# Kernel optimization log

Measured on AMD Instinct MI355X. Metric: run time of the kernel, lower is better.

The kernel has to match this reference:

```python
import jax, jax.numpy as jnp
import numpy as np

BETA = 0.25


def setup_inputs() -> dict:
    key = jax.random.key(0)
    k1, k2 = jax.random.split(key)
    B, W, H, C = 32, 64, 64, 64
    K = 512
    x = jax.random.normal(k1, (B, W, H, C), dtype=jnp.float32)
    # original uses random_uniform_initializer(0, 1)
    embedding = jax.random.uniform(k2, (K, C), dtype=jnp.float32)
    return {"x": x, "embedding": embedding}


def reference(x, embedding):
    B, W, H, C = x.shape
    K = embedding.shape[0]
    flat = x.reshape(-1, C)  # (N, C), N = B*W*H
    # squared L2 distance, expanded form (same math as sum((flat - emb)^2, -1))
    # avoids materializing the (N, K, C) tiled tensor of the original
    x2 = jnp.sum(flat * flat, axis=-1, keepdims=True)          # (N, 1)
    e2 = jnp.sum(embedding * embedding, axis=-1)               # (K,)
    cross = jnp.einsum('nc,kc->nk', flat, embedding)           # (N, K)
    dist = x2 - 2.0 * cross + e2[None, :]                      # (N, K)
    idx = jnp.argmin(dist, axis=-1).reshape(B, W, H)           # (B, W, H)
    quantized = embedding[idx]                                 # (B, W, H, C)
    embedding_loss = jnp.mean((jax.lax.stop_gradient(x) - quantized) ** 2)
    encoding_loss = jnp.mean((x - jax.lax.stop_gradient(quantized)) ** 2)
    loss = embedding_loss + BETA * encoding_loss
    # straight-through estimator
    quantized_ste = x + jax.lax.stop_gradient(quantized - x)
    return quantized_ste, loss
```

## Files before the change

kernel.cpp:

```cpp
#include <hip/hip_runtime.h>


#define C_DIM 64
#define K_EMB 512
#define NVEC (32 * 64 * 64)
#define BLK 512
#define VPW 64
#define NPB 512
#define GRID (NVEC / NPB)
#define KT (K_EMB / 16)
#define NT 4

typedef __attribute__((ext_vector_type(8))) short bf16x8;
typedef __attribute__((ext_vector_type(4))) float f32x4;

#define WS_E2   0
#define WS_EHI  4096
#define WS_ELO  (4096 + 65536)
#define WS_PART (4096 + 2 * 65536)

__device__ inline unsigned short f2bf(float f) {
    unsigned u = __float_as_uint(f);
    u += 0x7FFF + ((u >> 16) & 1);
    return (unsigned short)(u >> 16);
}
__device__ inline float bf2f(unsigned short h) {
    return __uint_as_float(((unsigned)h) << 16);
}
__device__ inline bool lessidx(float s, int i, float t, int j) {
    return (s < t) || (s == t && i < j);
}

__global__ __launch_bounds__(512) void vq_prep(const float* __restrict__ emb,
                                               float* __restrict__ e2,
                                               short* __restrict__ ehi,
                                               short* __restrict__ elo) {
    const int t = blockIdx.x * 512 + threadIdx.x;
    const int l = t & 63;
    const int kt2 = t >> 6;
    const int row = (kt2 >> 1) * 16 + (l & 15);
    const int cb  = (kt2 & 1) * 32 + (l >> 4) * 8;
    const float* src = emb + row * C_DIM + cb;
    bf16x8 vh, vl;
#pragma unroll
    for (int j = 0; j < 8; ++j) {
        float v = -2.0f * src[j];
        unsigned short h = f2bf(v);
        float hf = bf2f(h);
        unsigned short q = f2bf(v - hf);
        vh[j] = (short)h;
        vl[j] = (short)q;
    }
    *(bf16x8*)(ehi + (size_t)t * 8) = vh;
    *(bf16x8*)(elo + (size_t)t * 8) = vl;

    if (t < K_EMB) {
        const float* r = emb + t * C_DIM;
        float s = 0.f;
#pragma unroll
        for (int c = 0; c < C_DIM; ++c) s += r[c] * r[c];
        e2[t] = s;
    }
}

__global__ __launch_bounds__(BLK, 2) void vq_main(
    const float* __restrict__ x,
    const float* __restrict__ emb,
    const float* __restrict__ e2g,
    const short* __restrict__ ehi_g,
    const short* __restrict__ elo_g,
    float* __restrict__ out,
    double* __restrict__ partials)
{
    __shared__ __align__(16) short s_hi[K_EMB * C_DIM];
    __shared__ __align__(16) short s_lo[K_EMB * C_DIM];
    __shared__ __align__(16) float s_e2[K_EMB];
    __shared__ double s_wsum[BLK / 64];

    const int tid = threadIdx.x;

    {
        const float4* srch = (const float4*)ehi_g;
        const float4* srcl = (const float4*)elo_g;
        float4* dsth = (float4*)s_hi;
        float4* dstl = (float4*)s_lo;
#pragma unroll
        for (int i = 0; i < 16; ++i) dsth[tid + i * BLK] = srch[tid + i * BLK];
#pragma unroll
        for (int i = 0; i < 16; ++i) dstl[tid + i * BLK] = srcl[tid + i * BLK];
        if (tid < K_EMB) s_e2[tid] = e2g[tid];
    }
    __syncthreads();

    const int lane = tid & 63;
    const int wid  = tid >> 6;
    const int lr   = lane & 15;
    const int lh   = lane >> 4;
    const int nbase = blockIdx.x * NPB + wid * VPW;

    bf16x8 xh[NT][2], xl[NT][2];
    float x2p[NT];
#pragma unroll
    for (int nt = 0; nt < NT; ++nt) {
        const int n = nbase + nt * 16 + lr;
        const float* xp = x + (size_t)n * C_DIM;
        x2p[nt] = 0.f;
#pragma unroll
        for (int s = 0; s < 2; ++s) {
            const float* p = xp + s * 32 + lh * 8;
            float4 a = *(const float4*)(p);
            float4 b = *(const float4*)(p + 4);
            float vv[8] = {a.x, a.y, a.z, a.w, b.x, b.y, b.z, b.w};
#pragma unroll
            for (int j = 0; j < 8; ++j) {
                float v = vv[j];
                x2p[nt] += v * v;
                unsigned short h = f2bf(v);
                float hf = bf2f(h);
                unsigned short q = f2bf(v - hf);
                xh[nt][s][j] = (short)h;
                xl[nt][s][j] = (short)q;
            }
        }
    }

    float pb1[NT], pb2[NT];
#pragma unroll
    for (int nt = 0; nt < NT; ++nt) { pb1[nt] = 1e30f; pb2[nt] = 1e30f; }

    for (int kt = 0; kt < KT; ++kt) {
        const bf16x8* hp = (const bf16x8*)s_hi + kt * 128 + lane;
        const bf16x8* lp = (const bf16x8*)s_lo + kt * 128 + lane;
        bf16x8 ah0 = hp[0], ah1 = hp[64];
        bf16x8 al0 = lp[0], al1 = lp[64];
        float4 ev = *(const float4*)(s_e2 + kt * 16 + lh * 4);
        f32x4 a0 = {ev.x, ev.y, ev.z, ev.w};
        f32x4 a1 = a0, a2 = a0, a3 = a0;

        a0 = __builtin_amdgcn_mfma_f32_16x16x32_bf16(ah0, xh[0][0], a0, 0, 0, 0);
        a1 = __builtin_amdgcn_mfma_f32_16x16x32_bf16(ah0, xh[1][0], a1, 0, 0, 0);
        a2 = __builtin_amdgcn_mfma_f32_16x16x32_bf16(ah0, xh[2][0], a2, 0, 0, 0);
        a3 = __builtin_amdgcn_mfma_f32_16x16x32_bf16(ah0, xh[3][0], a3, 0, 0, 0);
        a0 = __builtin_amdgcn_mfma_f32_16x16x32_bf16(ah1, xh[0][1], a0, 0, 0, 0);
        a1 = __builtin_amdgcn_mfma_f32_16x16x32_bf16(ah1, xh[1][1], a1, 0, 0, 0);
        a2 = __builtin_amdgcn_mfma_f32_16x16x32_bf16(ah1, xh[2][1], a2, 0, 0, 0);
        a3 = __builtin_amdgcn_mfma_f32_16x16x32_bf16(ah1, xh[3][1], a3, 0, 0, 0);
        a0 = __builtin_amdgcn_mfma_f32_16x16x32_bf16(al0, xh[0][0], a0, 0, 0, 0);
        a1 = __builtin_amdgcn_mfma_f32_16x16x32_bf16(al0, xh[1][0], a1, 0, 0, 0);
        a2 = __builtin_amdgcn_mfma_f32_16x16x32_bf16(al0, xh[2][0], a2, 0, 0, 0);
        a3 = __builtin_amdgcn_mfma_f32_16x16x32_bf16(al0, xh[3][0], a3, 0, 0, 0);
        a0 = __builtin_amdgcn_mfma_f32_16x16x32_bf16(al1, xh[0][1], a0, 0, 0, 0);
        a1 = __builtin_amdgcn_mfma_f32_16x16x32_bf16(al1, xh[1][1], a1, 0, 0, 0);
        a2 = __builtin_amdgcn_mfma_f32_16x16x32_bf16(al1, xh[2][1], a2, 0, 0, 0);
        a3 = __builtin_amdgcn_mfma_f32_16x16x32_bf16(al1, xh[3][1], a3, 0, 0, 0);
        a0 = __builtin_amdgcn_mfma_f32_16x16x32_bf16(ah0, xl[0][0], a0, 0, 0, 0);
        a1 = __builtin_amdgcn_mfma_f32_16x16x32_bf16(ah0, xl[1][0], a1, 0, 0, 0);
        a2 = __builtin_amdgcn_mfma_f32_16x16x32_bf16(ah0, xl[2][0], a2, 0, 0, 0);
        a3 = __builtin_amdgcn_mfma_f32_16x16x32_bf16(ah0, xl[3][0], a3, 0, 0, 0);
        a0 = __builtin_amdgcn_mfma_f32_16x16x32_bf16(ah1, xl[0][1], a0, 0, 0, 0);
        a1 = __builtin_amdgcn_mfma_f32_16x16x32_bf16(ah1, xl[1][1], a1, 0, 0, 0);
        a2 = __builtin_amdgcn_mfma_f32_16x16x32_bf16(ah1, xl[2][1], a2, 0, 0, 0);
        a3 = __builtin_amdgcn_mfma_f32_16x16x32_bf16(ah1, xl[3][1], a3, 0, 0, 0);

        const unsigned kb4 = (unsigned)(kt * 4);
#define PACKMIN(ACC, NTI)                                                          \
        {                                                                          \
            unsigned q0 = ((__float_as_uint(ACC[0]) + 64u) & 0xFFFFFF80u) | (kb4 + 0); \
            unsigned q1 = ((__float_as_uint(ACC[1]) + 64u) & 0xFFFFFF80u) | (kb4 + 1); \
            unsigned q2 = ((__float_as_uint(ACC[2]) + 64u) & 0xFFFFFF80u) | (kb4 + 2); \
            unsigned q3 = ((__float_as_uint(ACC[3]) + 64u) & 0xFFFFFF80u) | (kb4 + 3); \
            float f0 = __uint_as_float(q0), f1 = __uint_as_float(q1);              \
            float f2 = __uint_as_float(q2), f3 = __uint_as_float(q3);              \
            float lo = fminf(f0, f1), hi = fmaxf(f0, f1);                          \
            pb2[NTI] = fminf(fminf(pb2[NTI], fmaxf(pb1[NTI], lo)), hi);            \
            pb1[NTI] = fminf(pb1[NTI], lo);                                        \
            lo = fminf(f2, f3); hi = fmaxf(f2, f3);                                \
            pb2[NTI] = fminf(fminf(pb2[NTI], fmaxf(pb1[NTI], lo)), hi);            \
            pb1[NTI] = fminf(pb1[NTI], lo);                                        \
        }
        PACKMIN(a0, 0)
        PACKMIN(a1, 1)
        PACKMIN(a2, 2)
        PACKMIN(a3, 3)
#undef PACKMIN
    }

    double dsum = 0.0;
#pragma unroll
    for (int nt = 0; nt < NT; ++nt) {
        unsigned u1 = __float_as_uint(pb1[nt]);
        unsigned u2 = __float_as_uint(pb2[nt]);
        int loc1 = u1 & 127, loc2 = u2 & 127;
        float b1 = __uint_as_float(u1 & 0xFFFFFF80u);
        float b2 = __uint_as_float(u2 & 0xFFFFFF80u);
        int i1 = ((loc1 >> 2) << 4) + lh * 4 + (loc1 & 3);
        int i2 = ((loc2 >> 2) << 4) + lh * 4 + (loc2 & 3);
        float xx = x2p[nt];
#pragma unroll
        for (int off = 16; off <= 32; off <<= 1) {
            float ob1 = __shfl_xor(b1, off, 64);
            int   oi1 = __shfl_xor(i1, off, 64);
            float ob2 = __shfl_xor(b2, off, 64);
            int   oi2 = __shfl_xor(i2, off, 64);
            float oxx = __shfl_xor(xx, off, 64);
            xx += oxx;
            bool to = lessidx(ob1, oi1, b1, i1);
            float w1 = to ? ob1 : b1;  int wi1 = to ? oi1 : i1;
            float l1 = to ? b1 : ob1;  int li1 = to ? i1 : oi1;
            float c2 = to ? ob2 : b2;  int ci2 = to ? oi2 : i2;
            bool t2 = lessidx(l1, li1, c2, ci2);
            b1 = w1; i1 = wi1;
            b2 = t2 ? l1 : c2; i2 = t2 ? li1 : ci2;
        }

        int bw = i1;
        if (lane < 16) {
            double md;
            if (b2 - b1 < 1.2e-2f) {
                const int n = nbase + nt * 16 + lane;
                const float4* xq = (const float4*)(x + (size_t)n * C_DIM);
                const float4* p1 = (const float4*)(emb + (size_t)i1 * C_DIM);
                const float4* p2 = (const float4*)(emb + (size_t)i2 * C_DIM);
                double s1 = 0.0, s2 = 0.0;
#pragma unroll
                for (int i = 0; i < 16; ++i) {
                    float4 xv = xq[i]; float4 a = p1[i]; float4 bq = p2[i];
                    double d;
                    d = (double)xv.x - (double)a.x;  s1 = fma(d, d, s1);
                    d = (double)xv.y - (double)a.y;  s1 = fma(d, d, s1);
                    d = (double)xv.z - (double)a.z;  s1 = fma(d, d, s1);
                    d = (double)xv.w - (double)a.w;  s1 = fma(d, d, s1);
                    d = (double)xv.x - (double)bq.x; s2 = fma(d, d, s2);
                    d = (double)xv.y - (double)bq.y; s2 = fma(d, d, s2);
                    d = (double)xv.z - (double)bq.z; s2 = fma(d, d, s2);
                    d = (double)xv.w - (double)bq.w; s2 = fma(d, d, s2);
                }
                if (s2 < s1 || (s1 == s2 && i2 < i1)) { bw = i2; md = s2; }
                else                                   { md = s1; }
            } else {
                md = (double)xx + (double)b1;
            }
            dsum += md;
        }

        {
            const int v  = lane >> 2;
            const int c0 = lane & 3;
            const int w  = __shfl(bw, v);
            const size_t rowb = ((size_t)(nbase + nt * 16 + v)) * 16;
            const float4* ep = (const float4*)emb + (size_t)w * 16;
            float4* op = (float4*)out;
#pragma unroll
            for (int it = 0; it < 4; ++it) op[rowb + c0 + it * 4] = ep[c0 + it * 4];
        }
    }

#pragma unroll
    for (int off = 1; off <= 8; off <<= 1) dsum += __shfl_xor(dsum, off, 64);
    if (lane == 0) s_wsum[wid] = dsum;
    __syncthreads();
    if (tid == 0) {
        double t = 0.0;
#pragma unroll
        for (int i = 0; i < BLK / 64; ++i) t += s_wsum[i];
        partials[blockIdx.x] = t;
    }
}

__global__ __launch_bounds__(256) void vq_finalize(const double* __restrict__ partials,
                                                   float* __restrict__ out) {
    double v = partials[threadIdx.x];
#pragma unroll
    for (int off = 32; off; off >>= 1) v += __shfl_down(v, off, 64);
    __shared__ double ls[4];
    const int lane = threadIdx.x & 63;
    const int wid  = threadIdx.x >> 6;
    if (lane == 0) ls[wid] = v;
    __syncthreads();
    if (threadIdx.x == 0) {
        double t = ls[0] + ls[1] + ls[2] + ls[3];
        double mean = t / (double)((size_t)NVEC * C_DIM);
        out[(size_t)NVEC * C_DIM] = (float)(1.25 * mean);
    }
}

extern "C" void kernel_launch(void* const* d_in, const int* in_sizes, int n_in,
                              void* d_out, int out_size, void* d_ws, size_t ws_size,
                              hipStream_t stream) {
    const float* x   = (const float*)d_in[0];
    const float* emb = (const float*)d_in[1];
    float* out = (float*)d_out;

    float*  e2       = (float*)((char*)d_ws + WS_E2);
    short*  ehi      = (short*)((char*)d_ws + WS_EHI);
    short*  elo      = (short*)((char*)d_ws + WS_ELO);
    double* partials = (double*)((char*)d_ws + WS_PART);

    vq_prep<<<8, 512, 0, stream>>>(emb, e2, ehi, elo);
    vq_main<<<GRID, BLK, 0, stream>>>(x, emb, e2, ehi, elo, out, partials);
    vq_finalize<<<1, 256, 0, stream>>>(partials, out);
}
```

Baseline: 51.83 us.

## Split per-wave vectors into two batches and prefetch the next batch and fragments

Each wave now handles its 64 vectors as two batches of 32 (NT=2), reusing the same k-loop and epilogue twice. The first batch's x rows are loaded before the codebook is staged into LDS, and the second batch's rows are loaded while the first batch is computed, so global load latency overlaps with work. The k-loop double-buffers the LDS codebook fragments one step ahead and is partially unrolled. The LDS staging loop is also cut from 16 to 8 iterations, which matches the shared-array size. This lowers accumulator register use, at the cost of reading the codebook fragments from LDS twice.

```diff
diff --git a/kernel.cpp b/kernel.cpp
--- a/kernel.cpp
+++ b/kernel.cpp
@@ -5,11 +5,11 @@
 #define K_EMB 512
 #define NVEC (32 * 64 * 64)
 #define BLK 512
-#define VPW 64
 #define NPB 512
+#define NBAT 256
 #define GRID (NVEC / NPB)
 #define KT (K_EMB / 16)
-#define NT 4
+#define NT 2
 
 typedef __attribute__((ext_vector_type(8))) short bf16x8;
 typedef __attribute__((ext_vector_type(4))) float f32x4;
@@ -63,53 +63,16 @@
     }
 }
 
-__global__ __launch_bounds__(BLK, 2) void vq_main(
-    const float* __restrict__ x,
-    const float* __restrict__ emb,
-    const float* __restrict__ e2g,
-    const short* __restrict__ ehi_g,
-    const short* __restrict__ elo_g,
-    float* __restrict__ out,
-    double* __restrict__ partials)
-{
-    __shared__ __align__(16) short s_hi[K_EMB * C_DIM];
-    __shared__ __align__(16) short s_lo[K_EMB * C_DIM];
-    __shared__ __align__(16) float s_e2[K_EMB];
-    __shared__ double s_wsum[BLK / 64];
-
-    const int tid = threadIdx.x;
-
-    {
-        const float4* srch = (const float4*)ehi_g;
-        const float4* srcl = (const float4*)elo_g;
-        float4* dsth = (float4*)s_hi;
-        float4* dstl = (float4*)s_lo;
-#pragma unroll
-        for (int i = 0; i < 16; ++i) dsth[tid + i * BLK] = srch[tid + i * BLK];
-#pragma unroll
-        for (int i = 0; i < 16; ++i) dstl[tid + i * BLK] = srcl[tid + i * BLK];
-        if (tid < K_EMB) s_e2[tid] = e2g[tid];
-    }
-    __syncthreads();
-
-    const int lane = tid & 63;
-    const int wid  = tid >> 6;
-    const int lr   = lane & 15;
-    const int lh   = lane >> 4;
-    const int nbase = blockIdx.x * NPB + wid * VPW;
-
-    bf16x8 xh[NT][2], xl[NT][2];
-    float x2p[NT];
+__device__ __forceinline__ void make_frags(const float4 xr[8],
+                                           bf16x8 xh[NT][2], bf16x8 xl[NT][2],
+                                           float x2p[NT]) {
 #pragma unroll
     for (int nt = 0; nt < NT; ++nt) {
-        const int n = nbase + nt * 16 + lr;
-        const float* xp = x + (size_t)n * C_DIM;
         x2p[nt] = 0.f;
 #pragma unroll
         for (int s = 0; s < 2; ++s) {
-            const float* p = xp + s * 32 + lh * 8;
-            float4 a = *(const float4*)(p);
-            float4 b = *(const float4*)(p + 4);
+            float4 a = xr[nt * 4 + s * 2 + 0];
+            float4 b = xr[nt * 4 + s * 2 + 1];
             float vv[8] = {a.x, a.y, a.z, a.w, b.x, b.y, b.z, b.w};
 #pragma unroll
             for (int j = 0; j < 8; ++j) {
@@ -123,44 +86,47 @@
             }
         }
     }
-
-    float pb1[NT], pb2[NT];
+}
+
+__device__ __forceinline__ void kloop(const short* s_hi, const short* s_lo,
+                                      const float* s_e2, int lane, int lh,
+                                      const bf16x8 xh[NT][2], const bf16x8 xl[NT][2],
+                                      float pb1[NT], float pb2[NT]) {
+    const bf16x8* hb = (const bf16x8*)s_hi + lane;
+    const bf16x8* lb = (const bf16x8*)s_lo + lane;
+    bf16x8 ah0 = hb[0], ah1 = hb[64];
+    bf16x8 al0 = lb[0], al1 = lb[64];
+    float4 ev = *(const float4*)(s_e2 + lh * 4);
+
 #pragma unroll
     for (int nt = 0; nt < NT; ++nt) { pb1[nt] = 1e30f; pb2[nt] = 1e30f; }
 
+#pragma unroll 4
     for (int kt = 0; kt < KT; ++kt) {
-        const bf16x8* hp = (const bf16x8*)s_hi + kt * 128 + lane;
-        const bf16x8* lp = (const bf16x8*)s_lo + kt * 128 + lane;
-        bf16x8 ah0 = hp[0], ah1 = hp[64];
-        bf16x8 al0 = lp[0], al1 = lp[64];
-        float4 ev = *(const float4*)(s_e2 + kt * 16 + lh * 4);
+        bf16x8 nh0 = ah0, nh1 = ah1, nl0 = al0, nl1 = al1;
+        float4 nev = ev;
+        if (kt + 1 < KT) {
+            nh0 = hb[(kt + 1) * 128];
+            nh1 = hb[(kt + 1) * 128 + 64];
+            nl0 = lb[(kt + 1) * 128];
+            nl1 = lb[(kt + 1) * 128 + 64];
+            nev = *(const float4*)(s_e2 + (kt + 1) * 16 + lh * 4);
+        }
+
         f32x4 a0 = {ev.x, ev.y, ev.z, ev.w};
-        f32x4 a1 = a0, a2 = a0, a3 = a0;
-
+        f32x4 a1 = a0;
         a0 = __builtin_amdgcn_mfma_f32_16x16x32_bf16(ah0, xh[0][0], a0, 0, 0, 0);
         a1 = __builtin_amdgcn_mfma_f32_16x16x32_bf16(ah0, xh[1][0], a1, 0, 0, 0);
-        a2 = __builtin_amdgcn_mfma_f32_16x16x32_bf16(ah0, xh[2][0], a2, 0, 0, 0);
-        a3 = __builtin_amdgcn_mfma_f32_16x16x32_bf16(ah0, xh[3][0], a3, 0, 0, 0);
         a0 = __builtin_amdgcn_mfma_f32_16x16x32_bf16(ah1, xh[0][1], a0, 0, 0, 0);
         a1 = __builtin_amdgcn_mfma_f32_16x16x32_bf16(ah1, xh[1][1], a1, 0, 0, 0);
-        a2 = __builtin_amdgcn_mfma_f32_16x16x32_bf16(ah1, xh[2][1], a2, 0, 0, 0);
-        a3 = __builtin_amdgcn_mfma_f32_16x16x32_bf16(ah1, xh[3][1], a3, 0, 0, 0);
         a0 = __builtin_amdgcn_mfma_f32_16x16x32_bf16(al0, xh[0][0], a0, 0, 0, 0);
         a1 = __builtin_amdgcn_mfma_f32_16x16x32_bf16(al0, xh[1][0], a1, 0, 0, 0);
-        a2 = __builtin_amdgcn_mfma_f32_16x16x32_bf16(al0, xh[2][0], a2, 0, 0, 0);
-        a3 = __builtin_amdgcn_mfma_f32_16x16x32_bf16(al0, xh[3][0], a3, 0, 0, 0);
         a0 = __builtin_amdgcn_mfma_f32_16x16x32_bf16(al1, xh[0][1], a0, 0, 0, 0);
         a1 = __builtin_amdgcn_mfma_f32_16x16x32_bf16(al1, xh[1][1], a1, 0, 0, 0);
-        a2 = __builtin_amdgcn_mfma_f32_16x16x32_bf16(al1, xh[2][1], a2, 0, 0, 0);
-        a3 = __builtin_amdgcn_mfma_f32_16x16x32_bf16(al1, xh[3][1], a3, 0, 0, 0);
         a0 = __builtin_amdgcn_mfma_f32_16x16x32_bf16(ah0, xl[0][0], a0, 0, 0, 0);
         a1 = __builtin_amdgcn_mfma_f32_16x16x32_bf16(ah0, xl[1][0], a1, 0, 0, 0);
-        a2 = __builtin_amdgcn_mfma_f32_16x16x32_bf16(ah0, xl[2][0], a2, 0, 0, 0);
-        a3 = __builtin_amdgcn_mfma_f32_16x16x32_bf16(ah0, xl[3][0], a3, 0, 0, 0);
         a0 = __builtin_amdgcn_mfma_f32_16x16x32_bf16(ah1, xl[0][1], a0, 0, 0, 0);
         a1 = __builtin_amdgcn_mfma_f32_16x16x32_bf16(ah1, xl[1][1], a1, 0, 0, 0);
-        a2 = __builtin_amdgcn_mfma_f32_16x16x32_bf16(ah1, xl[2][1], a2, 0, 0, 0);
-        a3 = __builtin_amdgcn_mfma_f32_16x16x32_bf16(ah1, xl[3][1], a3, 0, 0, 0);
 
         const unsigned kb4 = (unsigned)(kt * 4);
 #define PACKMIN(ACC, NTI)                                                          \
@@ -180,11 +146,17 @@
         }
         PACKMIN(a0, 0)
         PACKMIN(a1, 1)
-        PACKMIN(a2, 2)
-        PACKMIN(a3, 3)
 #undef PACKMIN
-    }
-
+        ah0 = nh0; ah1 = nh1; al0 = nl0; al1 = nl1; ev = nev;
+    }
+}
+
+__device__ __forceinline__ double epilogue(const float* __restrict__ x,
+                                           const float* __restrict__ emb,
+                                           float* __restrict__ out,
+                                           int nbase, int lane, int lh,
+                                           const float pb1[NT], const float pb2[NT],
+                                           const float x2p[NT]) {
     double dsum = 0.0;
 #pragma unroll
     for (int nt = 0; nt < NT; ++nt) {
@@ -254,6 +226,78 @@
             for (int it = 0; it < 4; ++it) op[rowb + c0 + it * 4] = ep[c0 + it * 4];
         }
     }
+    return dsum;
+}
+
+__global__ __launch_bounds__(BLK, 2) void vq_main(
+    const float* __restrict__ x,
+    const float* __restrict__ emb,
+    const float* __restrict__ e2g,
+    const short* __restrict__ ehi_g,
+    const short* __restrict__ elo_g,
+    float* __restrict__ out,
+    double* __restrict__ partials)
+{
+    __shared__ __align__(16) short s_hi[K_EMB * C_DIM];
+    __shared__ __align__(16) short s_lo[K_EMB * C_DIM];
+    __shared__ __align__(16) float s_e2[K_EMB];
+    __shared__ double s_wsum[BLK / 64];
+
+    const int tid  = threadIdx.x;
+    const int lane = tid & 63;
+    const int wid  = tid >> 6;
+    const int lr   = lane & 15;
+    const int lh   = lane >> 4;
+    const int nbase0 = blockIdx.x * NPB + wid * 32;
+    const int nbase1 = blockIdx.x * NPB + NBAT + wid * 32;
+
+    float4 xr0[8];
+#pragma unroll
+    for (int nt = 0; nt < NT; ++nt) {
+        const float* xp = x + (size_t)(nbase0 + nt * 16 + lr) * C_DIM;
+#pragma unroll
+        for (int s = 0; s < 2; ++s) {
+            xr0[nt * 4 + s * 2 + 0] = *(const float4*)(xp + s * 32 + lh * 8);
+            xr0[nt * 4 + s * 2 + 1] = *(const float4*)(xp + s * 32 + lh * 8 + 4);
+        }
+    }
+
+    {
+        const float4* srch = (const float4*)ehi_g;
+        const float4* srcl = (const float4*)elo_g;
+        float4* dsth = (float4*)s_hi;
+        float4* dstl = (float4*)s_lo;
+#pragma unroll
+        for (int i = 0; i < 8; ++i) dsth[tid + i * BLK] = srch[tid + i * BLK];
+#pragma unroll
+        for (int i = 0; i < 8; ++i) dstl[tid + i * BLK] = srcl[tid + i * BLK];
+        if (tid < K_EMB) s_e2[tid] = e2g[tid];
+    }
+    __syncthreads();
+
+    bf16x8 xh[NT][2], xl[NT][2];
+    float x2p0[NT];
+    make_frags(xr0, xh, xl, x2p0);
+
+    float4 xr1[8];
+#pragma unroll
+    for (int nt = 0; nt < NT; ++nt) {
+        const float* xp = x + (size_t)(nbase1 + nt * 16 + lr) * C_DIM;
+#pragma unroll
+        for (int s = 0; s < 2; ++s) {
+            xr1[nt * 4 + s * 2 + 0] = *(const float4*)(xp + s * 32 + lh * 8);
+            xr1[nt * 4 + s * 2 + 1] = *(const float4*)(xp + s * 32 + lh * 8 + 4);
+        }
+    }
+
+    float pb1[NT], pb2[NT];
+    kloop(s_hi, s_lo, s_e2, lane, lh, xh, xl, pb1, pb2);
+    double dsum = epilogue(x, emb, out, nbase0, lane, lh, pb1, pb2, x2p0);
+
+    float x2p1[NT];
+    make_frags(xr1, xh, xl, x2p1);
+    kloop(s_hi, s_lo, s_e2, lane, lh, xh, xl, pb1, pb2);
+    dsum += epilogue(x, emb, out, nbase1, lane, lh, pb1, pb2, x2p1);
 
 #pragma unroll
     for (int off = 1; off <= 8; off <<= 1) dsum += __shfl_xor(dsum, off, 64);
```

After: 50.66 us. 1.02x faster.

## Halve codebook LDS footprint via two-chunk staging and raise occupancy

Applied to the files above, without the earlier changes.

Stages the bf16 hi/lo codebook into shared memory in two halves of 256 entries instead of the full 512, cutting LDS per block from about 130KB to about 66KB. Each block now covers 256 vectors (2 tiles per wave), launch bounds rise to 4, and the grid and finalize kernel double to 512. The x loads are issued before the codebook copy so global latency overlaps it. The MFMA chain is split into three independent accumulators (hi*hi, lo*hi, hi*lo) that are summed at the end to shorten dependency chains. The cost is an extra mid-loop barrier and reload, and the codebook is re-read from global by twice as many blocks.

```diff
diff --git a/kernel.cpp b/kernel.cpp
--- a/kernel.cpp
+++ b/kernel.cpp
@@ -3,13 +3,13 @@
 
 #define C_DIM 64
 #define K_EMB 512
+#define KCH   (K_EMB / 2)
 #define NVEC (32 * 64 * 64)
 #define BLK 512
-#define VPW 64
-#define NPB 512
+#define NPB 256
 #define GRID (NVEC / NPB)
-#define KT (K_EMB / 16)
-#define NT 4
+#define KTC 16
+#define NT 2
 
 typedef __attribute__((ext_vector_type(8))) short bf16x8;
 typedef __attribute__((ext_vector_type(4))) float f32x4;
@@ -63,7 +63,7 @@
     }
 }
 
-__global__ __launch_bounds__(BLK, 2) void vq_main(
+__global__ __launch_bounds__(BLK, 4) void vq_main(
     const float* __restrict__ x,
     const float* __restrict__ emb,
     const float* __restrict__ e2g,
@@ -72,44 +72,51 @@
     float* __restrict__ out,
     double* __restrict__ partials)
 {
-    __shared__ __align__(16) short s_hi[K_EMB * C_DIM];
-    __shared__ __align__(16) short s_lo[K_EMB * C_DIM];
+    __shared__ __align__(16) short s_hi[KCH * C_DIM];
+    __shared__ __align__(16) short s_lo[KCH * C_DIM];
     __shared__ __align__(16) float s_e2[K_EMB];
     __shared__ double s_wsum[BLK / 64];
 
-    const int tid = threadIdx.x;
-
+    const int tid  = threadIdx.x;
+    const int lane = tid & 63;
+    const int wid  = tid >> 6;
+    const int lr   = lane & 15;
+    const int lh   = lane >> 4;
+    const int nbase = blockIdx.x * NPB + wid * 32;
+
+    float4 xr[8];
+#pragma unroll
+    for (int nt = 0; nt < NT; ++nt) {
+        const float* xp = x + (size_t)(nbase + nt * 16 + lr) * C_DIM;
+#pragma unroll
+        for (int s = 0; s < 2; ++s) {
+            xr[nt * 4 + s * 2 + 0] = *(const float4*)(xp + s * 32 + lh * 8);
+            xr[nt * 4 + s * 2 + 1] = *(const float4*)(xp + s * 32 + lh * 8 + 4);
+        }
+    }
+
+    if (tid < K_EMB) s_e2[tid] = e2g[tid];
     {
         const float4* srch = (const float4*)ehi_g;
         const float4* srcl = (const float4*)elo_g;
         float4* dsth = (float4*)s_hi;
         float4* dstl = (float4*)s_lo;
 #pragma unroll
-        for (int i = 0; i < 16; ++i) dsth[tid + i * BLK] = srch[tid + i * BLK];
-#pragma unroll
-        for (int i = 0; i < 16; ++i) dstl[tid + i * BLK] = srcl[tid + i * BLK];
-        if (tid < K_EMB) s_e2[tid] = e2g[tid];
+        for (int i = 0; i < 4; ++i) dsth[tid + i * BLK] = srch[tid + i * BLK];
+#pragma unroll
+        for (int i = 0; i < 4; ++i) dstl[tid + i * BLK] = srcl[tid + i * BLK];
     }
     __syncthreads();
-
-    const int lane = tid & 63;
-    const int wid  = tid >> 6;
-    const int lr   = lane & 15;
-    const int lh   = lane >> 4;
-    const int nbase = blockIdx.x * NPB + wid * VPW;
 
     bf16x8 xh[NT][2], xl[NT][2];
     float x2p[NT];
 #pragma unroll
     for (int nt = 0; nt < NT; ++nt) {
-        const int n = nbase + nt * 16 + lr;
-        const float* xp = x + (size_t)n * C_DIM;
         x2p[nt] = 0.f;
 #pragma unroll
         for (int s = 0; s < 2; ++s) {
-            const float* p = xp + s * 32 + lh * 8;
-            float4 a = *(const float4*)(p);
-            float4 b = *(const float4*)(p + 4);
+            float4 a = xr[nt * 4 + s * 2 + 0];
+            float4 b = xr[nt * 4 + s * 2 + 1];
             float vv[8] = {a.x, a.y, a.z, a.w, b.x, b.y, b.z, b.w};
 #pragma unroll
             for (int j = 0; j < 8; ++j) {
@@ -124,65 +131,73 @@
         }
     }
 
-    float pb1[NT], pb2[NT];
-#pragma unroll
-    for (int nt = 0; nt < NT; ++nt) { pb1[nt] = 1e30f; pb2[nt] = 1e30f; }
-
-    for (int kt = 0; kt < KT; ++kt) {
-        const bf16x8* hp = (const bf16x8*)s_hi + kt * 128 + lane;
-        const bf16x8* lp = (const bf16x8*)s_lo + kt * 128 + lane;
-        bf16x8 ah0 = hp[0], ah1 = hp[64];
-        bf16x8 al0 = lp[0], al1 = lp[64];
-        float4 ev = *(const float4*)(s_e2 + kt * 16 + lh * 4);
-        f32x4 a0 = {ev.x, ev.y, ev.z, ev.w};
-        f32x4 a1 = a0, a2 = a0, a3 = a0;
-
-        a0 = __builtin_amdgcn_mfma_f32_16x16x32_bf16(ah0, xh[0][0], a0, 0, 0, 0);
-        a1 = __builtin_amdgcn_mfma_f32_16x16x32_bf16(ah0, xh[1][0], a1, 0, 0, 0);
-        a2 = __builtin_amdgcn_mfma_f32_16x16x32_bf16(ah0, xh[2][0], a2, 0, 0, 0);
-        a3 = __builtin_amdgcn_mfma_f32_16x16x32_bf16(ah0, xh[3][0], a3, 0, 0, 0);
-        a0 = __builtin_amdgcn_mfma_f32_16x16x32_bf16(ah1, xh[0][1], a0, 0, 0, 0);
-        a1 = __builtin_amdgcn_mfma_f32_16x16x32_bf16(ah1, xh[1][1], a1, 0, 0, 0);
-        a2 = __builtin_amdgcn_mfma_f32_16x16x32_bf16(ah1, xh[2][1], a2, 0, 0, 0);
-        a3 = __builtin_amdgcn_mfma_f32_16x16x32_bf16(ah1, xh[3][1], a3, 0, 0, 0);
-        a0 = __builtin_amdgcn_mfma_f32_16x16x32_bf16(al0, xh[0][0], a0, 0, 0, 0);
-        a1 = __builtin_amdgcn_mfma_f32_16x16x32_bf16(al0, xh[1][0], a1, 0, 0, 0);
-        a2 = __builtin_amdgcn_mfma_f32_16x16x32_bf16(al0, xh[2][0], a2, 0, 0, 0);
-        a3 = __builtin_amdgcn_mfma_f32_16x16x32_bf16(al0, xh[3][0], a3, 0, 0, 0);
-        a0 = __builtin_amdgcn_mfma_f32_16x16x32_bf16(al1, xh[0][1], a0, 0, 0, 0);
-        a1 = __builtin_amdgcn_mfma_f32_16x16x32_bf16(al1, xh[1][1], a1, 0, 0, 0);
-        a2 = __builtin_amdgcn_mfma_f32_16x16x32_bf16(al1, xh[2][1], a2, 0, 0, 0);
-        a3 = __builtin_amdgcn_mfma_f32_16x16x32_bf16(al1, xh[3][1], a3, 0, 0, 0);
-        a0 = __builtin_amdgcn_mfma_f32_16x16x32_bf16(ah0, xl[0][0], a0, 0, 0, 0);
-        a1 = __builtin_amdgcn_mfma_f32_16x16x32_bf16(ah0, xl[1][0], a1, 0, 0, 0);
-        a2 = __builtin_amdgcn_mfma_f32_16x16x32_bf16(ah0, xl[2][0], a2, 0, 0, 0);
-        a3 = __builtin_amdgcn_mfma_f32_16x16x32_bf16(ah0, xl[3][0], a3, 0, 0, 0);
-        a0 = __builtin_amdgcn_mfma_f32_16x16x32_bf16(ah1, xl[0][1], a0, 0, 0, 0);
-        a1 = __builtin_amdgcn_mfma_f32_16x16x32_bf16(ah1, xl[1][1], a1, 0, 0, 0);
-        a2 = __builtin_amdgcn_mfma_f32_16x16x32_bf16(ah1, xl[2][1], a2, 0, 0, 0);
-        a3 = __builtin_amdgcn_mfma_f32_16x16x32_bf16(ah1, xl[3][1], a3, 0, 0, 0);
-
-        const unsigned kb4 = (unsigned)(kt * 4);
+    float pb1[NT] = {1e30f, 1e30f}, pb2[NT] = {1e30f, 1e30f};
+
+#pragma unroll 1
+    for (int ch = 0; ch < 2; ++ch) {
+        if (ch == 1) {
+            __syncthreads();
+            const float4* srch = (const float4*)ehi_g + 2048;
+            const float4* srcl = (const float4*)elo_g + 2048;
+            float4* dsth = (float4*)s_hi;
+            float4* dstl = (float4*)s_lo;
+#pragma unroll
+            for (int i = 0; i < 4; ++i) dsth[tid + i * BLK] = srch[tid + i * BLK];
+#pragma unroll
+            for (int i = 0; i < 4; ++i) dstl[tid + i * BLK] = srcl[tid + i * BLK];
+            __syncthreads();
+        }
+        const int ktb = ch * KTC;
+        const bf16x8* hb = (const bf16x8*)s_hi + lane;
+        const bf16x8* lb = (const bf16x8*)s_lo + lane;
+
+#pragma unroll 2
+        for (int kt = 0; kt < KTC; ++kt) {
+            bf16x8 ah0 = hb[kt * 128], ah1 = hb[kt * 128 + 64];
+            bf16x8 al0 = lb[kt * 128], al1 = lb[kt * 128 + 64];
+            float4 ev = *(const float4*)(s_e2 + (ktb + kt) * 16 + lh * 4);
+
+            f32x4 h0 = {ev.x, ev.y, ev.z, ev.w};
+            f32x4 h1 = h0;
+            f32x4 p0 = {0.f, 0.f, 0.f, 0.f};
+            f32x4 p1 = p0, q0 = p0, q1 = p0;
+
+            h0 = __builtin_amdgcn_mfma_f32_16x16x32_bf16(ah0, xh[0][0], h0, 0, 0, 0);
+            h1 = __builtin_amdgcn_mfma_f32_16x16x32_bf16(ah0, xh[1][0], h1, 0, 0, 0);
+            p0 = __builtin_amdgcn_mfma_f32_16x16x32_bf16(al0, xh[0][0], p0, 0, 0, 0);
+            p1 = __builtin_amdgcn_mfma_f32_16x16x32_bf16(al0, xh[1][0], p1, 0, 0, 0);
+            q0 = __builtin_amdgcn_mfma_f32_16x16x32_bf16(ah0, xl[0][0], q0, 0, 0, 0);
+            q1 = __builtin_amdgcn_mfma_f32_16x16x32_bf16(ah0, xl[1][0], q1, 0, 0, 0);
+            h0 = __builtin_amdgcn_mfma_f32_16x16x32_bf16(ah1, xh[0][1], h0, 0, 0, 0);
+            h1 = __builtin_amdgcn_mfma_f32_16x16x32_bf16(ah1, xh[1][1], h1, 0, 0, 0);
+            p0 = __builtin_amdgcn_mfma_f32_16x16x32_bf16(al1, xh[0][1], p0, 0, 0, 0);
+            p1 = __builtin_amdgcn_mfma_f32_16x16x32_bf16(al1, xh[1][1], p1, 0, 0, 0);
+            q0 = __builtin_amdgcn_mfma_f32_16x16x32_bf16(ah1, xl[0][1], q0, 0, 0, 0);
+            q1 = __builtin_amdgcn_mfma_f32_16x16x32_bf16(ah1, xl[1][1], q1, 0, 0, 0);
+
+            f32x4 s0 = (h0 + p0) + q0;
+            f32x4 s1 = (h1 + p1) + q1;
+
+            const unsigned kb4 = (unsigned)((ktb + kt) * 4);
 #define PACKMIN(ACC, NTI)                                                          \
-        {                                                                          \
-            unsigned q0 = ((__float_as_uint(ACC[0]) + 64u) & 0xFFFFFF80u) | (kb4 + 0); \
-            unsigned q1 = ((__float_as_uint(ACC[1]) + 64u) & 0xFFFFFF80u) | (kb4 + 1); \
-            unsigned q2 = ((__float_as_uint(ACC[2]) + 64u) & 0xFFFFFF80u) | (kb4 + 2); \
-            unsigned q3 = ((__float_as_uint(ACC[3]) + 64u) & 0xFFFFFF80u) | (kb4 + 3); \
-            float f0 = __uint_as_float(q0), f1 = __uint_as_float(q1);              \
-            float f2 = __uint_as_float(q2), f3 = __uint_as_float(q3);              \
-            float lo = fminf(f0, f1), hi = fmaxf(f0, f1);                          \
-            pb2[NTI] = fminf(fminf(pb2[NTI], fmaxf(pb1[NTI], lo)), hi);            \
-            pb1[NTI] = fminf(pb1[NTI], lo);                                        \
-            lo = fminf(f2, f3); hi = fmaxf(f2, f3);                                \
-            pb2[NTI] = fminf(fminf(pb2[NTI], fmaxf(pb1[NTI], lo)), hi);            \
-            pb1[NTI] = fminf(pb1[NTI], lo);                                        \
-        }
-        PACKMIN(a0, 0)
-        PACKMIN(a1, 1)
-        PACKMIN(a2, 2)
-        PACKMIN(a3, 3)
+            {                                                                      \
+                unsigned u0 = ((__float_as_uint(ACC[0]) + 64u) & 0xFFFFFF80u) | (kb4 + 0); \
+                unsigned u1 = ((__float_as_uint(ACC[1]) + 64u) & 0xFFFFFF80u) | (kb4 + 1); \
+                unsigned u2 = ((__float_as_uint(ACC[2]) + 64u) & 0xFFFFFF80u) | (kb4 + 2); \
+                unsigned u3 = ((__float_as_uint(ACC[3]) + 64u) & 0xFFFFFF80u) | (kb4 + 3); \
+                float f0 = __uint_as_float(u0), f1 = __uint_as_float(u1);          \
+                float f2 = __uint_as_float(u2), f3 = __uint_as_float(u3);          \
+                float lo = fminf(f0, f1), hi = fmaxf(f0, f1);                      \
+                pb2[NTI] = fminf(fminf(pb2[NTI], fmaxf(pb1[NTI], lo)), hi);        \
+                pb1[NTI] = fminf(pb1[NTI], lo);                                    \
+                lo = fminf(f2, f3); hi = fmaxf(f2, f3);                            \
+                pb2[NTI] = fminf(fminf(pb2[NTI], fmaxf(pb1[NTI], lo)), hi);        \
+                pb1[NTI] = fminf(pb1[NTI], lo);                                    \
+            }
+            PACKMIN(s0, 0)
+            PACKMIN(s1, 1)
 #undef PACKMIN
+        }
     }
 
     double dsum = 0.0;
@@ -267,18 +282,20 @@
     }
 }
 
-__global__ __launch_bounds__(256) void vq_finalize(const double* __restrict__ partials,
+__global__ __launch_bounds__(512) void vq_finalize(const double* __restrict__ partials,
                                                    float* __restrict__ out) {
     double v = partials[threadIdx.x];
 #pragma unroll
     for (int off = 32; off; off >>= 1) v += __shfl_down(v, off, 64);
-    __shared__ double ls[4];
+    __shared__ double ls[8];
     const int lane = threadIdx.x & 63;
     const int wid  = threadIdx.x >> 6;
     if (lane == 0) ls[wid] = v;
     __syncthreads();
     if (threadIdx.x == 0) {
-        double t = ls[0] + ls[1] + ls[2] + ls[3];
+        double t = 0.0;
+#pragma unroll
+        for (int i = 0; i < 8; ++i) t += ls[i];
         double mean = t / (double)((size_t)NVEC * C_DIM);
         out[(size_t)NVEC * C_DIM] = (float)(1.25 * mean);
     }
@@ -298,5 +315,5 @@
 
     vq_prep<<<8, 512, 0, stream>>>(emb, e2, ehi, elo);
     vq_main<<<GRID, BLK, 0, stream>>>(x, emb, e2, ehi, elo, out, partials);
-    vq_finalize<<<1, 256, 0, stream>>>(partials, out);
-}
+    vq_finalize<<<1, 512, 0, stream>>>(partials, out);
+}
```

After: 53.19 us. +2.6%, slower.

## Software-pipeline the codebook MFMA loop and prefetch x before the LDS fill

Applied to the files above, without the earlier changes.

Issues the global loads of each thread's x vectors before the codebook copy into shared memory, so their latency overlaps the LDS fill. Shrinks the codebook copy loops from 16 to 8 iterations per array. The old loops copied twice the array size and wrote past s_hi into s_lo. Restructures the main distance loop into a two-stage software pipeline with double-buffered fragments, so each tile's LDS loads and argmin packing interleave with the next tile's MFMAs. The cost is higher register pressure from holding prefetched x and two sets of fragments and accumulators, which could limit occupancy at two blocks per CU.

```diff
diff --git a/kernel.cpp b/kernel.cpp
--- a/kernel.cpp
+++ b/kernel.cpp
@@ -77,7 +77,23 @@
     __shared__ __align__(16) float s_e2[K_EMB];
     __shared__ double s_wsum[BLK / 64];
 
-    const int tid = threadIdx.x;
+    const int tid  = threadIdx.x;
+    const int lane = tid & 63;
+    const int wid  = tid >> 6;
+    const int lr   = lane & 15;
+    const int lh   = lane >> 4;
+    const int nbase = blockIdx.x * NPB + wid * VPW;
+
+    float4 xr[NT * 4];
+#pragma unroll
+    for (int nt = 0; nt < NT; ++nt) {
+        const float* xp = x + (size_t)(nbase + nt * 16 + lr) * C_DIM;
+#pragma unroll
+        for (int s = 0; s < 2; ++s) {
+            xr[nt * 4 + s * 2 + 0] = *(const float4*)(xp + s * 32 + lh * 8);
+            xr[nt * 4 + s * 2 + 1] = *(const float4*)(xp + s * 32 + lh * 8 + 4);
+        }
+    }
 
     {
         const float4* srch = (const float4*)ehi_g;
@@ -85,31 +101,22 @@
         float4* dsth = (float4*)s_hi;
         float4* dstl = (float4*)s_lo;
 #pragma unroll
-        for (int i = 0; i < 16; ++i) dsth[tid + i * BLK] = srch[tid + i * BLK];
-#pragma unroll
-        for (int i = 0; i < 16; ++i) dstl[tid + i * BLK] = srcl[tid + i * BLK];
+        for (int i = 0; i < 8; ++i) dsth[tid + i * BLK] = srch[tid + i * BLK];
+#pragma unroll
+        for (int i = 0; i < 8; ++i) dstl[tid + i * BLK] = srcl[tid + i * BLK];
         if (tid < K_EMB) s_e2[tid] = e2g[tid];
     }
     __syncthreads();
-
-    const int lane = tid & 63;
-    const int wid  = tid >> 6;
-    const int lr   = lane & 15;
-    const int lh   = lane >> 4;
-    const int nbase = blockIdx.x * NPB + wid * VPW;
 
     bf16x8 xh[NT][2], xl[NT][2];
     float x2p[NT];
 #pragma unroll
     for (int nt = 0; nt < NT; ++nt) {
-        const int n = nbase + nt * 16 + lr;
-        const float* xp = x + (size_t)n * C_DIM;
         x2p[nt] = 0.f;
 #pragma unroll
         for (int s = 0; s < 2; ++s) {
-            const float* p = xp + s * 32 + lh * 8;
-            float4 a = *(const float4*)(p);
-            float4 b = *(const float4*)(p + 4);
+            float4 a = xr[nt * 4 + s * 2 + 0];
+            float4 b = xr[nt * 4 + s * 2 + 1];
             float vv[8] = {a.x, a.y, a.z, a.w, b.x, b.y, b.z, b.w};
 #pragma unroll
             for (int j = 0; j < 8; ++j) {
@@ -124,66 +131,105 @@
         }
     }
 
-    float pb1[NT], pb2[NT];
-#pragma unroll
-    for (int nt = 0; nt < NT; ++nt) { pb1[nt] = 1e30f; pb2[nt] = 1e30f; }
-
-    for (int kt = 0; kt < KT; ++kt) {
-        const bf16x8* hp = (const bf16x8*)s_hi + kt * 128 + lane;
-        const bf16x8* lp = (const bf16x8*)s_lo + kt * 128 + lane;
-        bf16x8 ah0 = hp[0], ah1 = hp[64];
-        bf16x8 al0 = lp[0], al1 = lp[64];
-        float4 ev = *(const float4*)(s_e2 + kt * 16 + lh * 4);
-        f32x4 a0 = {ev.x, ev.y, ev.z, ev.w};
-        f32x4 a1 = a0, a2 = a0, a3 = a0;
-
-        a0 = __builtin_amdgcn_mfma_f32_16x16x32_bf16(ah0, xh[0][0], a0, 0, 0, 0);
-        a1 = __builtin_amdgcn_mfma_f32_16x16x32_bf16(ah0, xh[1][0], a1, 0, 0, 0);
-        a2 = __builtin_amdgcn_mfma_f32_16x16x32_bf16(ah0, xh[2][0], a2, 0, 0, 0);
-        a3 = __builtin_amdgcn_mfma_f32_16x16x32_bf16(ah0, xh[3][0], a3, 0, 0, 0);
-        a0 = __builtin_amdgcn_mfma_f32_16x16x32_bf16(ah1, xh[0][1], a0, 0, 0, 0);
-        a1 = __builtin_amdgcn_mfma_f32_16x16x32_bf16(ah1, xh[1][1], a1, 0, 0, 0);
-        a2 = __builtin_amdgcn_mfma_f32_16x16x32_bf16(ah1, xh[2][1], a2, 0, 0, 0);
-        a3 = __builtin_amdgcn_mfma_f32_16x16x32_bf16(ah1, xh[3][1], a3, 0, 0, 0);
-        a0 = __builtin_amdgcn_mfma_f32_16x16x32_bf16(al0, xh[0][0], a0, 0, 0, 0);
-        a1 = __builtin_amdgcn_mfma_f32_16x16x32_bf16(al0, xh[1][0], a1, 0, 0, 0);
-        a2 = __builtin_amdgcn_mfma_f32_16x16x32_bf16(al0, xh[2][0], a2, 0, 0, 0);
-        a3 = __builtin_amdgcn_mfma_f32_16x16x32_bf16(al0, xh[3][0], a3, 0, 0, 0);
-        a0 = __builtin_amdgcn_mfma_f32_16x16x32_bf16(al1, xh[0][1], a0, 0, 0, 0);
-        a1 = __builtin_amdgcn_mfma_f32_16x16x32_bf16(al1, xh[1][1], a1, 0, 0, 0);
-        a2 = __builtin_amdgcn_mfma_f32_16x16x32_bf16(al1, xh[2][1], a2, 0, 0, 0);
-        a3 = __builtin_amdgcn_mfma_f32_16x16x32_bf16(al1, xh[3][1], a3, 0, 0, 0);
-        a0 = __builtin_amdgcn_mfma_f32_16x16x32_bf16(ah0, xl[0][0], a0, 0, 0, 0);
-        a1 = __builtin_amdgcn_mfma_f32_16x16x32_bf16(ah0, xl[1][0], a1, 0, 0, 0);
-        a2 = __builtin_amdgcn_mfma_f32_16x16x32_bf16(ah0, xl[2][0], a2, 0, 0, 0);
-        a3 = __builtin_amdgcn_mfma_f32_16x16x32_bf16(ah0, xl[3][0], a3, 0, 0, 0);
-        a0 = __builtin_amdgcn_mfma_f32_16x16x32_bf16(ah1, xl[0][1], a0, 0, 0, 0);
-        a1 = __builtin_amdgcn_mfma_f32_16x16x32_bf16(ah1, xl[1][1], a1, 0, 0, 0);
-        a2 = __builtin_amdgcn_mfma_f32_16x16x32_bf16(ah1, xl[2][1], a2, 0, 0, 0);
-        a3 = __builtin_amdgcn_mfma_f32_16x16x32_bf16(ah1, xl[3][1], a3, 0, 0, 0);
-
-        const unsigned kb4 = (unsigned)(kt * 4);
-#define PACKMIN(ACC, NTI)                                                          \
-        {                                                                          \
-            unsigned q0 = ((__float_as_uint(ACC[0]) + 64u) & 0xFFFFFF80u) | (kb4 + 0); \
-            unsigned q1 = ((__float_as_uint(ACC[1]) + 64u) & 0xFFFFFF80u) | (kb4 + 1); \
-            unsigned q2 = ((__float_as_uint(ACC[2]) + 64u) & 0xFFFFFF80u) | (kb4 + 2); \
-            unsigned q3 = ((__float_as_uint(ACC[3]) + 64u) & 0xFFFFFF80u) | (kb4 + 3); \
-            float f0 = __uint_as_float(q0), f1 = __uint_as_float(q1);              \
-            float f2 = __uint_as_float(q2), f3 = __uint_as_float(q3);              \
-            float lo = fminf(f0, f1), hi = fmaxf(f0, f1);                          \
-            pb2[NTI] = fminf(fminf(pb2[NTI], fmaxf(pb1[NTI], lo)), hi);            \
-            pb1[NTI] = fminf(pb1[NTI], lo);                                        \
-            lo = fminf(f2, f3); hi = fmaxf(f2, f3);                                \
-            pb2[NTI] = fminf(fminf(pb2[NTI], fmaxf(pb1[NTI], lo)), hi);            \
-            pb1[NTI] = fminf(pb1[NTI], lo);                                        \
-        }
-        PACKMIN(a0, 0)
-        PACKMIN(a1, 1)
-        PACKMIN(a2, 2)
-        PACKMIN(a3, 3)
+    float pb1[NT] = {1e30f, 1e30f, 1e30f, 1e30f};
+    float pb2[NT] = {1e30f, 1e30f, 1e30f, 1e30f};
+
+    const bf16x8* hb = (const bf16x8*)s_hi + lane;
+    const bf16x8* lb = (const bf16x8*)s_lo + lane;
+
+#define MFMA16 __builtin_amdgcn_mfma_f32_16x16x32_bf16
+
+#define LOAD_FRAGS(KTI, FH0, FH1, FL0, FL1, EV)                  \
+    FH0 = hb[(KTI) * 128]; FH1 = hb[(KTI) * 128 + 64];           \
+    FL0 = lb[(KTI) * 128]; FL1 = lb[(KTI) * 128 + 64];           \
+    EV  = *(const f32x4*)(s_e2 + (KTI) * 16 + lh * 4);
+
+#define DO_MFMA(FH0, FH1, FL0, FL1, EV, C0, C1, C2, C3)          \
+    C0 = EV; C1 = EV; C2 = EV; C3 = EV;                          \
+    C0 = MFMA16(FH0, xh[0][0], C0, 0, 0, 0);                     \
+    C1 = MFMA16(FH0, xh[1][0], C1, 0, 0, 0);                     \
+    C2 = MFMA16(FH0, xh[2][0], C2, 0, 0, 0);                     \
+    C3 = MFMA16(FH0, xh[3][0], C3, 0, 0, 0);                     \
+    C0 = MFMA16(FH1, xh[0][1], C0, 0, 0, 0);                     \
+    C1 = MFMA16(FH1, xh[1][1], C1, 0, 0, 0);                     \
+    C2 = MFMA16(FH1, xh[2][1], C2, 0, 0, 0);                     \
+    C3 = MFMA16(FH1, xh[3][1], C3, 0, 0, 0);                     \
+    C0 = MFMA16(FL0, xh[0][0], C0, 0, 0, 0);                     \
+    C1 = MFMA16(FL0, xh[1][0], C1, 0, 0, 0);                     \
+    C2 = MFMA16(FL0, xh[2][0], C2, 0, 0, 0);                     \
+    C3 = MFMA16(FL0, xh[3][0], C3, 0, 0, 0);                     \
+    C0 = MFMA16(FL1, xh[0][1], C0, 0, 0, 0);                     \
+    C1 = MFMA16(FL1, xh[1][1], C1, 0, 0, 0);                     \
+    C2 = MFMA16(FL1, xh[2][1], C2, 0, 0, 0);                     \
+    C3 = MFMA16(FL1, xh[3][1], C3, 0, 0, 0);                     \
+    C0 = MFMA16(FH0, xl[0][0], C0, 0, 0, 0);                     \
+    C1 = MFMA16(FH0, xl[1][0], C1, 0, 0, 0);                     \
+    C2 = MFMA16(FH0, xl[2][0], C2, 0, 0, 0);                     \
+    C3 = MFMA16(FH0, xl[3][0], C3, 0, 0, 0);                     \
+    C0 = MFMA16(FH1, xl[0][1], C0, 0, 0, 0);                     \
+    C1 = MFMA16(FH1, xl[1][1], C1, 0, 0, 0);                     \
+    C2 = MFMA16(FH1, xl[2][1], C2, 0, 0, 0);                     \
+    C3 = MFMA16(FH1, xl[3][1], C3, 0, 0, 0);
+
+#define PACKMIN(ACC, NTI, KB4)                                                 \
+    {                                                                          \
+        unsigned q0 = ((__float_as_uint(ACC[0]) + 64u) & 0xFFFFFF80u) | (KB4 + 0); \
+        unsigned q1 = ((__float_as_uint(ACC[1]) + 64u) & 0xFFFFFF80u) | (KB4 + 1); \
+        unsigned q2 = ((__float_as_uint(ACC[2]) + 64u) & 0xFFFFFF80u) | (KB4 + 2); \
+        unsigned q3 = ((__float_as_uint(ACC[3]) + 64u) & 0xFFFFFF80u) | (KB4 + 3); \
+        float f0 = __uint_as_float(q0), f1 = __uint_as_float(q1);              \
+        float f2 = __uint_as_float(q2), f3 = __uint_as_float(q3);              \
+        float lo = fminf(f0, f1), hi = fmaxf(f0, f1);                          \
+        pb2[NTI] = fminf(fminf(pb2[NTI], fmaxf(pb1[NTI], lo)), hi);            \
+        pb1[NTI] = fminf(pb1[NTI], lo);                                        \
+        lo = fminf(f2, f3); hi = fmaxf(f2, f3);                                \
+        pb2[NTI] = fminf(fminf(pb2[NTI], fmaxf(pb1[NTI], lo)), hi);            \
+        pb1[NTI] = fminf(pb1[NTI], lo);                                        \
+    }
+
+    {
+        bf16x8 a0h0, a0h1, a0l0, a0l1;
+        bf16x8 a1h0, a1h1, a1l0, a1l1;
+        f32x4 ev0, ev1;
+        f32x4 c00, c01, c02, c03;
+        f32x4 c10, c11, c12, c13;
+
+        LOAD_FRAGS(0, a0h0, a0h1, a0l0, a0l1, ev0)
+        LOAD_FRAGS(1, a1h0, a1h1, a1l0, a1l1, ev1)
+        DO_MFMA(a0h0, a0h1, a0l0, a0l1, ev0, c00, c01, c02, c03)
+
+        for (int kt = 1; kt <= KT - 3; kt += 2) {
+            LOAD_FRAGS(kt + 1, a0h0, a0h1, a0l0, a0l1, ev0)
+            DO_MFMA(a1h0, a1h1, a1l0, a1l1, ev1, c10, c11, c12, c13)
+            {
+                const unsigned kb4 = (unsigned)((kt - 1) * 4);
+                PACKMIN(c00, 0, kb4) PACKMIN(c01, 1, kb4)
+                PACKMIN(c02, 2, kb4) PACKMIN(c03, 3, kb4)
+            }
+            LOAD_FRAGS(kt + 2, a1h0, a1h1, a1l0, a1l1, ev1)
+            DO_MFMA(a0h0, a0h1, a0l0, a0l1, ev0, c00, c01, c02, c03)
+            {
+                const unsigned kb4 = (unsigned)(kt * 4);
+                PACKMIN(c10, 0, kb4) PACKMIN(c11, 1, kb4)
+                PACKMIN(c12, 2, kb4) PACKMIN(c13, 3, kb4)
+            }
+        }
+        DO_MFMA(a1h0, a1h1, a1l0, a1l1, ev1, c10, c11, c12, c13)
+        {
+            const unsigned kb4 = (unsigned)((KT - 2) * 4);
+            PACKMIN(c00, 0, kb4) PACKMIN(c01, 1, kb4)
+            PACKMIN(c02, 2, kb4) PACKMIN(c03, 3, kb4)
+        }
+        {
+            const unsigned kb4 = (unsigned)((KT - 1) * 4);
+            PACKMIN(c10, 0, kb4) PACKMIN(c11, 1, kb4)
+            PACKMIN(c12, 2, kb4) PACKMIN(c13, 3, kb4)
+        }
+    }
 #undef PACKMIN
-    }
+#undef DO_MFMA
+#undef LOAD_FRAGS
+#undef MFMA16
 
     double dsum = 0.0;
 #pragma unroll
```

Measured after the change: 49.22 us. 5.0% less time.
